# Kernel optimization log

Measured on AMD Instinct MI355X. Metric: run time of the kernel, lower is better.

The kernel has to match this reference:

```python
import jax, jax.numpy as jnp
import numpy as np

EPS = 1e-5  # InstanceNorm2d default eps


def _branch(emb, Wq, K, Vt, Wo, kv_size):
    # emb: [b,n,c], Wq: [h,c,c] (nn.Linear weight, y = x @ W^T)
    # Qt: [b,h,c,n] = stack_h(emb @ Wq[h]^T).transpose(-1,-2)
    Qt = jnp.einsum('bnc,hdc->bhdn', emb, Wq)
    scores = jnp.einsum('bhdn,bhnk->bhdk', Qt, K) / jnp.sqrt(jnp.float32(kv_size))
    # InstanceNorm2d over heads channel: normalize each [c,kv] map per (b,h), no affine
    m = scores.mean(axis=(-2, -1), keepdims=True)
    v = scores.var(axis=(-2, -1), keepdims=True)
    scores = (scores - m) * jax.lax.rsqrt(v + EPS)
    probs = jax.nn.softmax(scores, axis=-1)            # [b,h,c,kv]
    ctx = jnp.einsum('bhdk,bhkn->bhdn', probs, Vt)     # [b,h,c,n]
    ctx = ctx.mean(axis=1).transpose(0, 2, 1)          # mean over heads -> [b,n,c]
    return ctx @ Wo.T


def setup_inputs() -> dict:
    key = jax.random.key(0)
    ks = jax.random.split(key, 15)
    B, N, H, KV = 16, 196, 4, 960
    C = [64, 128, 256, 512]
    inp = {}
    for i, c in enumerate(C):
        inp[f'emb{i+1}'] = jax.random.normal(ks[i], (B, N, c), jnp.float32)
    inp['emb_all'] = jax.random.normal(ks[4], (B, N, KV), jnp.float32)
    for i, c in enumerate(C):
        inp[f'Wq{i+1}'] = jax.random.normal(ks[5 + i], (H, c, c), jnp.float32) / np.sqrt(c)
    inp['Wk'] = jax.random.normal(ks[9], (H, KV, KV), jnp.float32) / np.sqrt(KV)
    inp['Wv'] = jax.random.normal(ks[10], (H, KV, KV), jnp.float32) / np.sqrt(KV)
    for i, c in enumerate(C):
        inp[f'Wo{i+1}'] = jax.random.normal(ks[11 + i], (c, c), jnp.float32) / np.sqrt(c)
    return inp


def reference(emb1, emb2, emb3, emb4, emb_all,
              Wq1, Wq2, Wq3, Wq4, Wk, Wv, Wo1, Wo2, Wo3, Wo4):
    KV = emb_all.shape[-1]
    # per-head shared K and V: [b,h,n,kv]; Vt = V.transpose(-1,-2): [b,h,kv,n]
    K = jnp.einsum('bnk,hok->bhno', emb_all, Wk)
    Vt = jnp.einsum('bnk,hok->bhon', emb_all, Wv)
    O1 = _branch(emb1, Wq1, K, Vt, Wo1, KV)
    O2 = _branch(emb2, Wq2, K, Vt, Wo2, KV)
    O3 = _branch(emb3, Wq3, K, Vt, Wo3, KV)
    O4 = _branch(emb4, Wq4, K, Vt, Wo4, KV)
    return (O1, O2, O3, O4)
```

## Files before the change

kernel.cpp:

```cpp
#include <hip/hip_runtime.h>
#include <math.h>

#define BB 16
#define NP 196
#define HH 4
#define KVD 960
#define KP 224

typedef __attribute__((ext_vector_type(8))) short s8v;
typedef __attribute__((ext_vector_type(8))) unsigned short u8v;
typedef __attribute__((ext_vector_type(4))) unsigned short u4v;
typedef __attribute__((ext_vector_type(4))) float f4v;

static inline int divup(int a, int b){ return (a+b-1)/b; }
static inline int imin(int a, int b){ return a < b ? a : b; }

__device__ __forceinline__ unsigned short bf16r(float x){
    unsigned int u = __float_as_uint(x);
    u += 0x7fffu + ((u >> 16) & 1u);
    return (unsigned short)(u >> 16);
}
__device__ __forceinline__ float bf16f(unsigned short h){
    return __uint_as_float(((unsigned int)h) << 16);
}

__device__ __forceinline__ void gload16(const unsigned short* g, unsigned short* l){
    __builtin_amdgcn_global_load_lds(
        (const __attribute__((address_space(1))) void*)g,
        (__attribute__((address_space(3))) void*)l, 16, 0, 0);
}

struct DecTable {
    const float* src[15];
    unsigned short* dh[15];
    unsigned short* dl[15];
    long n4[15];
};

__global__ __launch_bounds__(256)
void decomp_all(DecTable T)
{
    int seg = blockIdx.y;
    const float* x = T.src[seg];
    unsigned short* hi = T.dh[seg];
    unsigned short* lo = T.dl[seg];
    long n4 = T.n4[seg];
    for (long i = (long)blockIdx.x * 256 + threadIdx.x; i < n4; i += (long)gridDim.x * 256) {
        float4 v = ((const float4*)x)[i];
        float a[4] = {v.x, v.y, v.z, v.w};
        u4v h, l;
#pragma unroll
        for (int e = 0; e < 4; e++) {
            unsigned short hb = bf16r(a[e]);
            h[e] = hb;
            l[e] = bf16r(a[e] - bf16f(hb));
        }
        *(u4v*)(hi + i * 4) = h;
        *(u4v*)(lo + i * 4) = l;
    }
}

template<int OSPLIT, int STATS>
__global__ __launch_bounds__(256)
void gemm_split(const unsigned short* __restrict__ Ah, const unsigned short* __restrict__ Al,
                const unsigned short* __restrict__ Bh, const unsigned short* __restrict__ Bl,
                float* __restrict__ Cf, unsigned short* __restrict__ Ch,
                unsigned short* __restrict__ Cl, double* __restrict__ part,
                int M, int Nn, int Kk, int ldA, int ldB, int ldC,
                long sAb, long sAh_, long sBb, long sBh_, long sCb, long sCh_,
                int Hdiv, float alpha)
{
    __shared__ u8v AsV[128 * 8];
    __shared__ u8v BsV[128 * 8];
    unsigned short* As = (unsigned short*)AsV;
    unsigned short* Bs = (unsigned short*)BsV;

    int z  = blockIdx.z;
    int bb = z / Hdiv, hz = z - bb * Hdiv;
    const unsigned short* gah = Ah + (long)bb * sAb + (long)hz * sAh_;
    const unsigned short* gal = Al + (long)bb * sAb + (long)hz * sAh_;
    const unsigned short* gbh = Bh + (long)bb * sBb + (long)hz * sBh_;
    const unsigned short* gbl = Bl + (long)bb * sBb + (long)hz * sBh_;
    long coff = (long)bb * sCb + (long)hz * sCh_;

    int t = threadIdx.x;
    int m0 = blockIdx.y * 128, n0 = blockIdx.x * 128;
    int wave = t >> 6, lane = t & 63;
    int wm = wave >> 1, wn = wave & 1;
    int lr = lane & 15, lk = lane >> 4;

    int ls   = (lane & 7) ^ (lane >> 3);
    int comp = ls >> 2;
    int chnk = ls & 3;
    const unsigned short* gA = comp ? gal : gah;
    const unsigned short* gB = comp ? gbl : gbh;
    const unsigned short* aptr[4];
    const unsigned short* bptr[4];
#pragma unroll
    for (int j = 0; j < 4; j++) {
        int ra = m0 + wave * 32 + j * 8 + (lane >> 3);
        ra = (ra < M) ? ra : (M - 1);
        aptr[j] = gA + (long)ra * ldA + chnk * 8;
        int rb = n0 + wave * 32 + j * 8 + (lane >> 3);
        rb = (rb < Nn) ? rb : (Nn - 1);
        bptr[j] = gB + (long)rb * ldB + chnk * 8;
    }

    f4v acc[4][4];
#pragma unroll
    for (int i = 0; i < 4; i++)
#pragma unroll
        for (int j = 0; j < 4; j++) acc[i][j] = (f4v){0.f, 0.f, 0.f, 0.f};

    int nkt = Kk >> 5;
    for (int kt = 0; kt < nkt; ++kt) {
        int k0 = kt << 5;
#pragma unroll
        for (int j = 0; j < 4; j++) {
            gload16(aptr[j] + k0, As + (wave * 4 + j) * 512);
            gload16(bptr[j] + k0, Bs + (wave * 4 + j) * 512);
        }
        __syncthreads();

        s8v afh[4], afl[4], bfh[4], bfl[4];
#pragma unroll
        for (int i = 0; i < 4; i++) {
            int rw = wm * 64 + i * 16 + lr;
            afh[i] = *(const s8v*)&As[rw * 64 + ((lk ^ (rw & 7)) << 3)];
            afl[i] = *(const s8v*)&As[rw * 64 + (((lk + 4) ^ (rw & 7)) << 3)];
            int cw = wn * 64 + i * 16 + lr;
            bfh[i] = *(const s8v*)&Bs[cw * 64 + ((lk ^ (cw & 7)) << 3)];
            bfl[i] = *(const s8v*)&Bs[cw * 64 + (((lk + 4) ^ (cw & 7)) << 3)];
        }
#pragma unroll
        for (int i = 0; i < 4; i++)
#pragma unroll
            for (int j = 0; j < 4; j++) {
                acc[i][j] = __builtin_amdgcn_mfma_f32_16x16x32_bf16(afh[i], bfh[j], acc[i][j], 0, 0, 0);
                acc[i][j] = __builtin_amdgcn_mfma_f32_16x16x32_bf16(afl[i], bfh[j], acc[i][j], 0, 0, 0);
                acc[i][j] = __builtin_amdgcn_mfma_f32_16x16x32_bf16(afh[i], bfl[j], acc[i][j], 0, 0, 0);
            }
        __syncthreads();
    }

    float s1 = 0.f, s2 = 0.f;
#pragma unroll
    for (int i = 0; i < 4; i++)
#pragma unroll
        for (int j = 0; j < 4; j++)
#pragma unroll
            for (int r = 0; r < 4; r++) {
                int gr = m0 + wm * 64 + i * 16 + lk * 4 + r;
                int gc = n0 + wn * 64 + j * 16 + lr;
                if (gr < M) {
                    if (gc < Nn) {
                        float v = acc[i][j][r] * alpha;
                        if (STATS) { s1 += v; s2 += v * v; }
                        if (OSPLIT) {
                            unsigned short hb = bf16r(v);
                            Ch[coff + (long)gr * ldC + gc] = hb;
                            Cl[coff + (long)gr * ldC + gc] = bf16r(v - bf16f(hb));
                        } else {
                            Cf[coff + (long)gr * ldC + gc] = v;
                        }
                    } else if (OSPLIT && gc < ldC) {
                        Ch[coff + (long)gr * ldC + gc] = 0;
                        Cl[coff + (long)gr * ldC + gc] = 0;
                    }
                }
            }

    if (STATS) {
        double* sh = (double*)AsV;
        sh[t] = (double)s1; sh[256 + t] = (double)s2;
        __syncthreads();
        for (int o = 128; o > 0; o >>= 1) {
            if (t < o) { sh[t] += sh[t + o]; sh[256 + t] += sh[256 + t + o]; }
            __syncthreads();
        }
        if (t == 0) {
            int slot = blockIdx.x + (int)gridDim.x * blockIdx.y;
            part[(long)z * 64 + slot * 2 + 0] = sh[0];
            part[(long)z * 64 + slot * 2 + 1] = sh[256];
        }
    }
}

__global__ __launch_bounds__(256)
void pv_fused(const float* __restrict__ Sb, const unsigned short* __restrict__ Vh,
              const unsigned short* __restrict__ Vl, const double* __restrict__ part,
              float* __restrict__ Cb, int c, int m0, int nslot)
{
    __shared__ unsigned short As[64 * 64];
    __shared__ unsigned short Bs[224 * 64];
    __shared__ float Zlds[64];
    __shared__ float bc2[2];

    int z  = blockIdx.z;
    int gm = m0 + z;
    int my0 = blockIdx.y * 64;

    int t = threadIdx.x;
    int wave = t >> 6, lane = t & 63;
    int wm = wave >> 1, wn = wave & 1;
    int lr = lane & 15, lk = lane >> 4;

    if (t == 0) {
        const double* pp = part + (long)gm * 64;
        double su = 0.0, sq = 0.0;
        for (int q = 0; q < nslot; q++) { su += pp[q * 2]; sq += pp[q * 2 + 1]; }
        float inv_e = 1.0f / (float)(c * KVD);
        float mean = (float)(su * (double)inv_e);
        float var  = (float)(sq * (double)inv_e) - mean * mean;
        float is   = rsqrtf(var + 1e-5f);
        bc2[0] = is; bc2[1] = -mean * is;
    }
    __syncthreads();
    float is = bc2[0], dd = bc2[1];

    int arow = t >> 2, achk = t & 3;
    const float* sp = Sb + (size_t)z * c * KVD + (size_t)(my0 + arow) * KVD + achk * 8;
    unsigned short* awh = &As[arow * 64 + (( achk      ^ (arow & 7)) << 3)];
    unsigned short* awl = &As[arow * 64 + (((achk + 4) ^ (arow & 7)) << 3)];

    int ls   = (lane & 7) ^ (lane >> 3);
    int comp = ls >> 2, chnk = ls & 3;
    const unsigned short* vbase = (comp ? Vl : Vh) + (long)gm * (196L * KVD);
    const unsigned short* bptr[7];
    unsigned short* bdst[7];
#pragma unroll
    for (int q = 0; q < 7; q++) {
        int rlog = (wave * 7 + q) * 8 + (lane >> 3);
        int vrow = (rlog < NP) ? rlog : (NP - 1);
        bptr[q] = vbase + (long)vrow * KVD + chnk * 8;
        bdst[q] = &Bs[(wave * 7 + q) * 512];
    }

    f4v acc[2][7];
#pragma unroll
    for (int i = 0; i < 2; i++)
#pragma unroll
        for (int j = 0; j < 7; j++) acc[i][j] = (f4v){0.f, 0.f, 0.f, 0.f};
    float zp = 0.f;

    for (int kt = 0; kt < 30; ++kt) {
        int k0 = kt << 5;
#pragma unroll
        for (int q = 0; q < 7; q++) gload16(bptr[q] + k0, bdst[q]);

        float4 v0 = *(const float4*)(sp + k0);
        float4 v1 = *(const float4*)(sp + k0 + 4);
        float s[8] = {v0.x, v0.y, v0.z, v0.w, v1.x, v1.y, v1.z, v1.w};
        u8v hv, lv;
#pragma unroll
        for (int e = 0; e < 8; e++) {
            float p = __expf(fmaf(s[e], is, dd));
            zp += p;
            unsigned short hb = bf16r(p);
            hv[e] = hb;
            lv[e] = bf16r(p - bf16f(hb));
        }
        *(u8v*)awh = hv;
        *(u8v*)awl = lv;
        __syncthreads();

        s8v afh[2], afl[2], bfh[7], bfl[7];
#pragma unroll
        for (int i = 0; i < 2; i++) {
            int ar = wm * 32 + i * 16 + lr;
            afh[i] = *(const s8v*)&As[ar * 64 + ((lk ^ (ar & 7)) << 3)];
            afl[i] = *(const s8v*)&As[ar * 64 + (((lk + 4) ^ (ar & 7)) << 3)];
        }
#pragma unroll
        for (int j = 0; j < 7; j++) {
            int br = wn * 112 + j * 16 + lr;
            bfh[j] = *(const s8v*)&Bs[br * 64 + ((lk ^ (br & 7)) << 3)];
            bfl[j] = *(const s8v*)&Bs[br * 64 + (((lk + 4) ^ (br & 7)) << 3)];
        }
#pragma unroll
        for (int i = 0; i < 2; i++)
#pragma unroll
            for (int j = 0; j < 7; j++) {
                acc[i][j] = __builtin_amdgcn_mfma_f32_16x16x32_bf16(afh[i], bfh[j], acc[i][j], 0, 0, 0);
                acc[i][j] = __builtin_amdgcn_mfma_f32_16x16x32_bf16(afl[i], bfh[j], acc[i][j], 0, 0, 0);
                acc[i][j] = __builtin_amdgcn_mfma_f32_16x16x32_bf16(afh[i], bfl[j], acc[i][j], 0, 0, 0);
            }
        __syncthreads();
    }

    zp += __shfl_xor(zp, 1);
    zp += __shfl_xor(zp, 2);
    if ((t & 3) == 0) Zlds[arow] = zp;
    __syncthreads();

    float rz[2][4];
#pragma unroll
    for (int i = 0; i < 2; i++)
#pragma unroll
        for (int r = 0; r < 4; r++)
            rz[i][r] = 1.0f / Zlds[wm * 32 + i * 16 + lk * 4 + r];

    float* co = Cb + (size_t)gm * c * NP;
#pragma unroll
    for (int i = 0; i < 2; i++)
#pragma unroll
        for (int j = 0; j < 7; j++)
#pragma unroll
            for (int r = 0; r < 4; r++) {
                int grl = wm * 32 + i * 16 + lk * 4 + r;
                int gc  = wn * 112 + j * 16 + lr;
                if (gc < NP)
                    co[(size_t)(my0 + grl) * NP + gc] = acc[i][j][r] * rz[i][r];
            }
}

__global__ __launch_bounds__(256)
void mean_t_kernel(const float* __restrict__ Cb, unsigned short* __restrict__ Mh,
                   unsigned short* __restrict__ Ml, int c)
{
    int b  = blockIdx.z;
    int n0 = blockIdx.x * 32;
    int d0 = blockIdx.y * 32;
    __shared__ float tile[32][33];
    int tx = threadIdx.x & 31;
    int ty = threadIdx.x >> 5;
#pragma unroll
    for (int i = 0; i < 4; i++) {
        int d = d0 + ty + i * 8;
        int n = n0 + tx;
        float s = 0.f;
        if (n < NP) {
#pragma unroll
            for (int h = 0; h < HH; h++)
                s += Cb[(((long)(b * HH + h)) * c + d) * NP + n];
        }
        tile[ty + i * 8][tx] = 0.25f * s;
    }
    __syncthreads();
#pragma unroll
    for (int i = 0; i < 4; i++) {
        int n = n0 + ty + i * 8;
        int d = d0 + tx;
        if (n < NP) {
            float val = tile[tx][ty + i * 8];
            long idx = ((long)b * NP + n) * c + d;
            unsigned short hb = bf16r(val);
            Mh[idx] = hb;
            Ml[idx] = bf16r(val - bf16f(hb));
        }
    }
}

extern "C" void kernel_launch(void* const* d_in, const int* in_sizes, int n_in,
                              void* d_out, int out_size, void* d_ws, size_t ws_size,
                              hipStream_t stream)
{
    const float* embf[4] = {(const float*)d_in[0], (const float*)d_in[1],
                            (const float*)d_in[2], (const float*)d_in[3]};
    const float* emb_all = (const float*)d_in[4];
    const float* Wq[4]   = {(const float*)d_in[5], (const float*)d_in[6],
                            (const float*)d_in[7], (const float*)d_in[8]};
    const float* Wk = (const float*)d_in[9];
    const float* Wv = (const float*)d_in[10];
    const float* Wo[4]   = {(const float*)d_in[11], (const float*)d_in[12],
                            (const float*)d_in[13], (const float*)d_in[14]};
    float* out = (float*)d_out;

    const int Cc[4] = {64, 128, 256, 512};

    char* base = (char*)d_ws;
    size_t off = 0;
    auto carve = [&](size_t bytes) -> void* {
        void* p = base + off;
        off = (off + bytes + 255) & ~(size_t)255;
        return p;
    };

    const long NEA   = (long)BB * NP * KVD;
    const long NWKV  = (long)HH * KVD * KVD;
    const long SUMC2 = 64L*64 + 128L*128 + 256L*256 + 512L*512;

    unsigned short* wkH = (unsigned short*)carve(NWKV * 2);
    unsigned short* wkL = (unsigned short*)carve(NWKV * 2);
    unsigned short* wvH = (unsigned short*)carve(NWKV * 2);
    unsigned short* wvL = (unsigned short*)carve(NWKV * 2);
    unsigned short* wqH = (unsigned short*)carve((long)HH * SUMC2 * 2);
    unsigned short* wqL = (unsigned short*)carve((long)HH * SUMC2 * 2);
    unsigned short* woH = (unsigned short*)carve(SUMC2 * 2);
    unsigned short* woL = (unsigned short*)carve(SUMC2 * 2);
    unsigned short* eaH = (unsigned short*)carve(NEA * 2);
    unsigned short* eaL = (unsigned short*)carve(NEA * 2);
    unsigned short* eiH = (unsigned short*)carve(NEA * 2);
    unsigned short* eiL = (unsigned short*)carve(NEA * 2);
    double* part = (double*)carve(64L * 64 * 8);

    size_t fixed_off = off;
    auto group_bytes = [&](int gb) -> size_t {
        long nbh = (long)gb * HH;
        size_t s = 0;
        auto add = [&](size_t b){ s += (b + 255) & ~(size_t)255; };
        add(nbh * KVD * KP * 2); add(nbh * KVD * KP * 2);
        add(nbh * NP * KVD * 2); add(nbh * NP * KVD * 2);
        add(nbh * 512 * KP * 2); add(nbh * 512 * KP * 2);
        add(nbh * 512 * NP * 4);
        add((long)gb * NP * 512 * 2); add((long)gb * NP * 512 * 2);
        return s;
    };
    const size_t minchunk = (size_t)512 * KVD * 4 + (1 << 20);
    int GB = 16;
    while (GB > 1 && fixed_off + group_bytes(GB) + minchunk > ws_size) GB >>= 1;
    const long NBH = (long)GB * HH;

    unsigned short* KtH = (unsigned short*)carve(NBH * KVD * KP * 2);
    unsigned short* KtL = (unsigned short*)carve(NBH * KVD * KP * 2);
    unsigned short* VH  = (unsigned short*)carve(NBH * NP * KVD * 2);
    unsigned short* VL  = (unsigned short*)carve(NBH * NP * KVD * 2);
    unsigned short* QtH = (unsigned short*)carve(NBH * 512 * KP * 2);
    unsigned short* QtL = (unsigned short*)carve(NBH * 512 * KP * 2);
    float*  Cb          = (float*)carve(NBH * 512 * NP * 4);
    unsigned short* MbH = (unsigned short*)carve((long)GB * NP * 512 * 2);
    unsigned short* MbL = (unsigned short*)carve((long)GB * NP * 512 * 2);

    size_t savail = (ws_size > off) ? (ws_size - off) : 0;
    char* chunk = base + off;

    dim3 blk(256);
    const float alphaS = 1.0f / sqrtf((float)KVD);

    long eio[4], wqo[4], woo[4];
    { long eo = 0, qo = 0, oo = 0;
      for (int i = 0; i < 4; i++) {
          eio[i] = eo; eo += (long)BB * NP * Cc[i];
          wqo[i] = qo; qo += (long)HH * Cc[i] * Cc[i];
          woo[i] = oo; oo += (long)Cc[i] * Cc[i];
      } }
    {
        DecTable T;
        int k = 0;
        for (int i = 0; i < 4; i++) {
            T.src[k] = embf[i]; T.dh[k] = eiH + eio[i]; T.dl[k] = eiL + eio[i];
            T.n4[k] = ((long)BB * NP * Cc[i]) / 4; k++;
        }
        T.src[k] = emb_all; T.dh[k] = eaH; T.dl[k] = eaL; T.n4[k] = NEA / 4; k++;
        for (int i = 0; i < 4; i++) {
            T.src[k] = Wq[i]; T.dh[k] = wqH + wqo[i]; T.dl[k] = wqL + wqo[i];
            T.n4[k] = ((long)HH * Cc[i] * Cc[i]) / 4; k++;
        }
        T.src[k] = Wk; T.dh[k] = wkH; T.dl[k] = wkL; T.n4[k] = NWKV / 4; k++;
        T.src[k] = Wv; T.dh[k] = wvH; T.dl[k] = wvL; T.n4[k] = NWKV / 4; k++;
        for (int i = 0; i < 4; i++) {
            T.src[k] = Wo[i]; T.dh[k] = woH + woo[i]; T.dl[k] = woL + woo[i];
            T.n4[k] = ((long)Cc[i] * Cc[i]) / 4; k++;
        }
        decomp_all<<<dim3(512, 15, 1), blk, 0, stream>>>(T);
    }

    long obase[4];
    { long o = 0; for (int i = 0; i < 4; i++) { obase[i] = o; o += (long)BB * NP * Cc[i]; } }

    for (int g0 = 0; g0 < BB; g0 += GB) {
        const unsigned short* eaHg = eaH + (long)g0 * NP * KVD;
        const unsigned short* eaLg = eaL + (long)g0 * NP * KVD;

        gemm_split<1,0><<<dim3(2, 8, (int)NBH), blk, 0, stream>>>(
            wkH, wkL, eaHg, eaLg, nullptr, KtH, KtL, nullptr,
            KVD, NP, KVD, KVD, KVD, KP,
            0, (long)KVD * KVD, (long)NP * KVD, 0,
            (long)HH * KVD * KP, (long)KVD * KP, HH, 1.0f);

        gemm_split<1,0><<<dim3(8, 2, (int)NBH), blk, 0, stream>>>(
            eaHg, eaLg, wvH, wvL, nullptr, VH, VL, nullptr,
            NP, KVD, KVD, KVD, KVD, KVD,
            (long)NP * KVD, 0, 0, (long)KVD * KVD,
            (long)HH * NP * KVD, (long)NP * KVD, HH, 1.0f);

        for (int i = 0; i < 4; i++) {
            int c = Cc[i];

            gemm_split<1,0><<<dim3(2, divup(HH * c, 128), GB), blk, 0, stream>>>(
                wqH + wqo[i], wqL + wqo[i],
                eiH + eio[i] + (long)g0 * NP * c, eiL + eio[i] + (long)g0 * NP * c,
                nullptr, QtH, QtL, nullptr,
                HH * c, NP, c, c, c, KP,
                0, 0, (long)NP * c, 0,
                (long)HH * c * KP, 0, 1, 1.0f);

            int nslot = 8 * divup(c, 128);

            size_t per = (size_t)c * KVD * 4;
            int G = (savail >= per) ? (int)(savail / per) : 1;
            if (G > (int)NBH) G = (int)NBH;
            if (G < 1) G = 1;
            float* Sb = (float*)chunk;

            for (int m0 = 0; m0 < (int)NBH; m0 += G) {
                int g = imin(G, (int)NBH - m0);
                gemm_split<0,1><<<dim3(8, divup(c, 128), g), blk, 0, stream>>>(
                    QtH + (size_t)m0 * c * KP, QtL + (size_t)m0 * c * KP,
                    KtH + (size_t)m0 * KVD * KP, KtL + (size_t)m0 * KVD * KP,
                    Sb, nullptr, nullptr, part + (size_t)m0 * 64,
                    c, KVD, KP, KP, KP, KVD,
                    (long)c * KP, 0, (long)KVD * KP, 0, (long)c * KVD, 0,
                    1, alphaS);
                pv_fused<<<dim3(1, c / 64, g), blk, 0, stream>>>(
                    Sb, VH, VL, part, Cb, c, m0, nslot);
            }
            mean_t_kernel<<<dim3(divup(NP, 32), c / 32, GB), blk, 0, stream>>>(Cb, MbH, MbL, c);
            gemm_split<0,0><<<dim3(divup(c, 128), divup(GB * NP, 128), 1), blk, 0, stream>>>(
                MbH, MbL, woH + woo[i], woL + woo[i],
                out + obase[i] + (long)g0 * NP * c, nullptr, nullptr, nullptr,
                GB * NP, c, c, c, c, c,
                0, 0, 0, 0, 0, 0, 1, 1.0f);
        }
    }
}
```

Before: 1.113 ms.

## Store attention scores as fp16, shrink K padding, and reuse score chunk for emb_all

The QK^T score buffer now holds fp16 values instead of fp32. This halves the bytes written by the score GEMM and read by the fused softmax·V kernel. The K-transpose leading dimension drops from 224 to 200 to cut padding traffic. The emb_all split buffers now live in the score chunk when the workspace allows it, which lets the whole batch run as one group. Scores lose precision, fp16 has a smaller mantissa than fp32, and the K GEMM reads past the 200-wide rows into the 512-byte tail pad, so tolerance and correctness risk both rise.

```diff
diff --git a/kernel.cpp b/kernel.cpp
--- a/kernel.cpp
+++ b/kernel.cpp
@@ -1,4 +1,5 @@
 #include <hip/hip_runtime.h>
+#include <hip/hip_fp16.h>
 #include <math.h>
 
 #define BB 16
@@ -6,6 +7,7 @@
 #define HH 4
 #define KVD 960
 #define KP 224
+#define LDK 200
 
 typedef __attribute__((ext_vector_type(8))) short s8v;
 typedef __attribute__((ext_vector_type(8))) unsigned short u8v;
@@ -60,7 +62,7 @@
     }
 }
 
-template<int OSPLIT, int STATS>
+template<int OUTK, int STATS>
 __global__ __launch_bounds__(256)
 void gemm_split(const unsigned short* __restrict__ Ah, const unsigned short* __restrict__ Al,
                 const unsigned short* __restrict__ Bh, const unsigned short* __restrict__ Bl,
@@ -156,14 +158,19 @@
                     if (gc < Nn) {
                         float v = acc[i][j][r] * alpha;
                         if (STATS) { s1 += v; s2 += v * v; }
-                        if (OSPLIT) {
+                        if (OUTK == 1) {
                             unsigned short hb = bf16r(v);
                             Ch[coff + (long)gr * ldC + gc] = hb;
                             Cl[coff + (long)gr * ldC + gc] = bf16r(v - bf16f(hb));
+                        } else if (OUTK == 2) {
+                            __half hh = __float2half(v);
+                            unsigned short us;
+                            __builtin_memcpy(&us, &hh, 2);
+                            Ch[coff + (long)gr * ldC + gc] = us;
                         } else {
                             Cf[coff + (long)gr * ldC + gc] = v;
                         }
-                    } else if (OSPLIT && gc < ldC) {
+                    } else if (OUTK == 1 && gc < ldC) {
                         Ch[coff + (long)gr * ldC + gc] = 0;
                         Cl[coff + (long)gr * ldC + gc] = 0;
                     }
@@ -187,7 +194,7 @@
 }
 
 __global__ __launch_bounds__(256)
-void pv_fused(const float* __restrict__ Sb, const unsigned short* __restrict__ Vh,
+void pv_fused(const unsigned short* __restrict__ Sb, const unsigned short* __restrict__ Vh,
               const unsigned short* __restrict__ Vl, const double* __restrict__ part,
               float* __restrict__ Cb, int c, int m0, int nslot)
 {
@@ -219,7 +226,7 @@
     float is = bc2[0], dd = bc2[1];
 
     int arow = t >> 2, achk = t & 3;
-    const float* sp = Sb + (size_t)z * c * KVD + (size_t)(my0 + arow) * KVD + achk * 8;
+    const unsigned short* sp = Sb + (size_t)z * c * KVD + (size_t)(my0 + arow) * KVD + achk * 8;
     unsigned short* awh = &As[arow * 64 + (( achk      ^ (arow & 7)) << 3)];
     unsigned short* awl = &As[arow * 64 + (((achk + 4) ^ (arow & 7)) << 3)];
 
@@ -248,13 +255,14 @@
 #pragma unroll
         for (int q = 0; q < 7; q++) gload16(bptr[q] + k0, bdst[q]);
 
-        float4 v0 = *(const float4*)(sp + k0);
-        float4 v1 = *(const float4*)(sp + k0 + 4);
-        float s[8] = {v0.x, v0.y, v0.z, v0.w, v1.x, v1.y, v1.z, v1.w};
+        u8v sv = *(const u8v*)(sp + k0);
         u8v hv, lv;
 #pragma unroll
         for (int e = 0; e < 8; e++) {
-            float p = __expf(fmaf(s[e], is, dd));
+            __half hh;
+            unsigned short us = sv[e];
+            __builtin_memcpy(&hh, &us, 2);
+            float p = __expf(fmaf(__half2float(hh), is, dd));
             zp += p;
             unsigned short hb = bf16r(p);
             hv[e] = hb;
@@ -370,9 +378,10 @@
 
     char* base = (char*)d_ws;
     size_t off = 0;
+    auto align256 = [](size_t b) -> size_t { return (b + 255) & ~(size_t)255; };
     auto carve = [&](size_t bytes) -> void* {
         void* p = base + off;
-        off = (off + bytes + 255) & ~(size_t)255;
+        off += align256(bytes);
         return p;
     };
 
@@ -388,31 +397,45 @@
     unsigned short* wqL = (unsigned short*)carve((long)HH * SUMC2 * 2);
     unsigned short* woH = (unsigned short*)carve(SUMC2 * 2);
     unsigned short* woL = (unsigned short*)carve(SUMC2 * 2);
-    unsigned short* eaH = (unsigned short*)carve(NEA * 2);
-    unsigned short* eaL = (unsigned short*)carve(NEA * 2);
     unsigned short* eiH = (unsigned short*)carve(NEA * 2);
     unsigned short* eiL = (unsigned short*)carve(NEA * 2);
     double* part = (double*)carve(64L * 64 * 8);
 
     size_t fixed_off = off;
+    const size_t eaBytes = 2 * align256(NEA * 2);
+
     auto group_bytes = [&](int gb) -> size_t {
         long nbh = (long)gb * HH;
         size_t s = 0;
-        auto add = [&](size_t b){ s += (b + 255) & ~(size_t)255; };
-        add(nbh * KVD * KP * 2); add(nbh * KVD * KP * 2);
+        auto add = [&](size_t b){ s += align256(b); };
+        add(nbh * KVD * LDK * 2 + 512); add(nbh * KVD * LDK * 2 + 512);
         add(nbh * NP * KVD * 2); add(nbh * NP * KVD * 2);
         add(nbh * 512 * KP * 2); add(nbh * 512 * KP * 2);
         add(nbh * 512 * NP * 4);
         add((long)gb * NP * 512 * 2); add((long)gb * NP * 512 * 2);
         return s;
     };
-    const size_t minchunk = (size_t)512 * KVD * 4 + (1 << 20);
-    int GB = 16;
-    while (GB > 1 && fixed_off + group_bytes(GB) + minchunk > ws_size) GB >>= 1;
+
+    int GB;
+    bool eaChunk;
+    if (fixed_off + group_bytes(16) + eaBytes + (2u << 20) <= ws_size) {
+        GB = 16; eaChunk = true;
+    } else {
+        eaChunk = false;
+        const size_t minchunk = (size_t)512 * KVD * 2 + (1u << 20);
+        GB = 8;
+        while (GB > 1 && fixed_off + eaBytes + group_bytes(GB) + minchunk > ws_size) GB >>= 1;
+    }
+    unsigned short* eaH = nullptr;
+    unsigned short* eaL = nullptr;
+    if (!eaChunk) {
+        eaH = (unsigned short*)carve(NEA * 2);
+        eaL = (unsigned short*)carve(NEA * 2);
+    }
     const long NBH = (long)GB * HH;
 
-    unsigned short* KtH = (unsigned short*)carve(NBH * KVD * KP * 2);
-    unsigned short* KtL = (unsigned short*)carve(NBH * KVD * KP * 2);
+    unsigned short* KtH = (unsigned short*)carve(NBH * KVD * LDK * 2 + 512);
+    unsigned short* KtL = (unsigned short*)carve(NBH * KVD * LDK * 2 + 512);
     unsigned short* VH  = (unsigned short*)carve(NBH * NP * KVD * 2);
     unsigned short* VL  = (unsigned short*)carve(NBH * NP * KVD * 2);
     unsigned short* QtH = (unsigned short*)carve(NBH * 512 * KP * 2);
@@ -421,8 +444,12 @@
     unsigned short* MbH = (unsigned short*)carve((long)GB * NP * 512 * 2);
     unsigned short* MbL = (unsigned short*)carve((long)GB * NP * 512 * 2);
 
+    char* chunk = base + off;
     size_t savail = (ws_size > off) ? (ws_size - off) : 0;
-    char* chunk = base + off;
+    if (eaChunk) {
+        eaH = (unsigned short*)chunk;
+        eaL = (unsigned short*)(chunk + align256(NEA * 2));
+    }
 
     dim3 blk(256);
     const float alphaS = 1.0f / sqrtf((float)KVD);
@@ -464,9 +491,9 @@
 
         gemm_split<1,0><<<dim3(2, 8, (int)NBH), blk, 0, stream>>>(
             wkH, wkL, eaHg, eaLg, nullptr, KtH, KtL, nullptr,
-            KVD, NP, KVD, KVD, KVD, KP,
+            KVD, NP, KVD, KVD, KVD, LDK,
             0, (long)KVD * KVD, (long)NP * KVD, 0,
-            (long)HH * KVD * KP, (long)KVD * KP, HH, 1.0f);
+            (long)HH * KVD * LDK, (long)KVD * LDK, HH, 1.0f);
 
         gemm_split<1,0><<<dim3(8, 2, (int)NBH), blk, 0, stream>>>(
             eaHg, eaLg, wvH, wvL, nullptr, VH, VL, nullptr,
@@ -487,20 +514,20 @@
 
             int nslot = 8 * divup(c, 128);
 
-            size_t per = (size_t)c * KVD * 4;
+            size_t per = (size_t)c * KVD * 2;
             int G = (savail >= per) ? (int)(savail / per) : 1;
             if (G > (int)NBH) G = (int)NBH;
             if (G < 1) G = 1;
-            float* Sb = (float*)chunk;
+            unsigned short* Sb = (unsigned short*)chunk;
 
             for (int m0 = 0; m0 < (int)NBH; m0 += G) {
                 int g = imin(G, (int)NBH - m0);
-                gemm_split<0,1><<<dim3(8, divup(c, 128), g), blk, 0, stream>>>(
+                gemm_split<2,1><<<dim3(8, divup(c, 128), g), blk, 0, stream>>>(
                     QtH + (size_t)m0 * c * KP, QtL + (size_t)m0 * c * KP,
-                    KtH + (size_t)m0 * KVD * KP, KtL + (size_t)m0 * KVD * KP,
-                    Sb, nullptr, nullptr, part + (size_t)m0 * 64,
-                    c, KVD, KP, KP, KP, KVD,
-                    (long)c * KP, 0, (long)KVD * KP, 0, (long)c * KVD, 0,
+                    KtH + (size_t)m0 * KVD * LDK, KtL + (size_t)m0 * KVD * LDK,
+                    nullptr, Sb, nullptr, part + (size_t)m0 * 64,
+                    c, KVD, KP, KP, LDK, KVD,
+                    (long)c * KP, 0, (long)KVD * LDK, 0, (long)c * KVD, 0,
                     1, alphaS);
                 pv_fused<<<dim3(1, c / 64, g), blk, 0, stream>>>(
                     Sb, VH, VL, part, Cb, c, m0, nslot);
```

New measurement: 972.8 us. -12.6%, faster.
